# Optimization experiments

Hardware: AMD Instinct MI355X
Metric: run time of the kernel (lower is better)

The kernel has to match this reference:

```python
import jax, jax.numpy as jnp
import numpy as np

B, T, D_K, N_HEADS, D_FF, VOCAB, N_LAYERS = 4, 1024, 1024, 16, 4096, 65, 6


def setup_inputs() -> dict:
    key = jax.random.key(0)
    ks = jax.random.split(key, 12)
    f = lambda k, sh: jax.random.normal(k, sh, dtype=jnp.float32) * 0.02
    return {
        "batchData": jax.random.randint(ks[0], (B, T), 0, VOCAB),
        "target": jax.random.randint(ks[1], (B, T), 0, VOCAB),
        "pos": jnp.arange(T),
        "Wtok": f(ks[2], (VOCAB, D_K)),
        "Wpos": f(ks[3], (T, D_K)),
        "Wq": f(ks[4], (D_K, D_K)), "bq": jnp.zeros((D_K,), jnp.float32),
        "Wk": f(ks[5], (D_K, D_K)), "bk": jnp.zeros((D_K,), jnp.float32),
        "Wv": f(ks[6], (D_K, D_K)), "bv": jnp.zeros((D_K,), jnp.float32),
        "W1": f(ks[7], (D_K, D_FF)), "b1": jnp.zeros((D_FF,), jnp.float32),
        "W2": f(ks[8], (D_FF, D_K)), "b2": jnp.zeros((D_K,), jnp.float32),
        "ln_w": jnp.ones((D_K,), jnp.float32),
        "Wf": f(ks[9], (D_K, VOCAB)), "bf": jnp.zeros((VOCAB,), jnp.float32),
        "n_layers": N_LAYERS,
        "n_heads": N_HEADS,
    }


def layer_norm(x, w, eps=1e-5):
    m = jnp.mean(x, axis=-1, keepdims=True)
    v = jnp.var(x, axis=-1, keepdims=True)
    return (x - m) / jnp.sqrt(v + eps) * w


def reference(batchData, target, pos, Wtok, Wpos, Wq, bq, Wk, bk, Wv, bv,
              W1, b1, W2, b2, ln_w, Wf, bf, n_layers, n_heads):
    x = Wtok[batchData] + Wpos[pos]  # [B, T, C] (pos embedding broadcasts)
    Bsz, Tlen, C = x.shape
    dh = C // n_heads
    mask = jnp.tril(jnp.ones((Tlen, Tlen), dtype=bool))
    inv_sqrt_dk = 1.0 / jnp.sqrt(jnp.float32(C))  # source divides by sqrt(full d_k)

    def block(x):
        q = (x @ Wq + bq).reshape(Bsz, Tlen, n_heads, dh).transpose(0, 2, 1, 3)
        k = (x @ Wk + bk).reshape(Bsz, Tlen, n_heads, dh).transpose(0, 2, 1, 3)
        v = (x @ Wv + bv).reshape(Bsz, Tlen, n_heads, dh).transpose(0, 2, 1, 3)
        scores = jnp.einsum('bhqd,bhkd->bhqk', q, k) * inv_sqrt_dk
        scores = jnp.where(mask, scores, -jnp.inf)
        attn = jax.nn.softmax(scores, axis=-1)
        h = jnp.einsum('bhqk,bhkd->bhqd', attn, v)
        h = h.transpose(0, 2, 1, 3).reshape(Bsz, Tlen, C)
        h = h + layer_norm(h, ln_w)           # x = x + ln(x) (shared ln)
        ff = jax.nn.relu(h @ W1 + b1) @ W2 + b2
        return ff + layer_norm(ff, ln_w)      # same shared ln again

    # ModuleList repeats the SAME block object, so weights are shared across layers
    for _ in range(n_layers):
        x = block(x)

    logits = x @ Wf + bf                       # [B, T, V]
    probs = jax.nn.softmax(logits, axis=1)     # softmax over T, as in source
    pred = probs.reshape(Bsz * Tlen, -1)
    onehot = jax.nn.one_hot(target.reshape(-1), VOCAB, dtype=jnp.float32)
    # F.cross_entropy with soft (one-hot float) targets
    loss = -jnp.mean(jnp.sum(onehot * jax.nn.log_softmax(pred, axis=-1), axis=-1))
    return loss, probs
```

## Files before the change

kernel.cpp:

```cpp
#include <hip/hip_runtime.h>

typedef __attribute__((ext_vector_type(8))) short bh8;
typedef __attribute__((ext_vector_type(4))) float f4v;

constexpr int VOC = 65;
constexpr int NL  = 6;
constexpr int Mrow = 4096;

__device__ inline float b2f(unsigned short u) {
  union { unsigned int i; float f; } x; x.i = ((unsigned int)u) << 16; return x.f;
}
__device__ inline unsigned short f2b(float f) {
  union { float f; unsigned int i; } x; x.f = f;
  return (unsigned short)((x.i + 0x7FFFu + ((x.i >> 16) & 1u)) >> 16);
}
__device__ inline void gld16(const void* g, void* l) {
  __builtin_amdgcn_global_load_lds(
      (const __attribute__((address_space(1))) unsigned int*)g,
      (__attribute__((address_space(3))) unsigned int*)l, 16, 0, 0);
}
__device__ inline bh8 lds_swz(const unsigned short* base, int row, int colbyte) {
  int off = row * 128 + (colbyte ^ ((row & 7) << 4));
  return *(const bh8*)((const char*)base + off);
}
__device__ inline f4v mfma16(bh8 a, bh8 b, f4v c) {
  return __builtin_amdgcn_mfma_f32_16x16x32_bf16(a, b, c, 0, 0, 0);
}
#define WAITV(n) asm volatile("s_waitcnt vmcnt(" #n ")" ::: "memory")
template <int N> __device__ inline void waitvl() {
  if constexpr (N == 0)
    asm volatile("s_waitcnt vmcnt(0) lgkmcnt(0)" ::: "memory");
  else if constexpr (N == 3)
    asm volatile("s_waitcnt vmcnt(3) lgkmcnt(0)" ::: "memory");
  else if constexpr (N == 4)
    asm volatile("s_waitcnt vmcnt(4) lgkmcnt(0)" ::: "memory");
  else
    asm volatile("s_waitcnt vmcnt(6) lgkmcnt(0)" ::: "memory");
}

__global__ __launch_bounds__(256) void wt_conv(const float* __restrict__ src,
    unsigned short* __restrict__ dst, int K, int N) {
  __shared__ float t[32][33];
  int k0 = blockIdx.x * 32, n0 = blockIdx.y * 32;
  int tid = threadIdx.x;
#pragma unroll
  for (int i = 0; i < 4; ++i) {
    int idx = tid + i * 256;
    int kr = idx >> 5, nc = idx & 31;
    t[kr][nc] = (n0 + nc < N) ? src[(size_t)(k0 + kr) * N + n0 + nc] : 0.f;
  }
  __syncthreads();
#pragma unroll
  for (int i = 0; i < 4; ++i) {
    int idx = tid + i * 256;
    int nr = idx >> 5, kc = idx & 31;
    dst[(size_t)(n0 + nr) * K + k0 + kc] = f2b(t[kc][nr]);
  }
}

__global__ __launch_bounds__(256) void bias_prep(
    const float* __restrict__ bq, const float* __restrict__ bk,
    const float* __restrict__ bv, const float* __restrict__ bf,
    float* __restrict__ bqkv, float* __restrict__ bfp) {
  int i = blockIdx.x * 256 + threadIdx.x;
  if (i < 1024) bqkv[i] = bq[i];
  else if (i < 2048) bqkv[i] = bk[i - 1024];
  else if (i < 3072) bqkv[i] = bv[i - 2048];
  else if (i < 3200) bfp[i - 3072] = (i - 3072 < VOC) ? bf[i - 3072] : 0.f;
}

__global__ __launch_bounds__(256) void embed_bf(const int* __restrict__ tok,
    const float* __restrict__ Wtok, const float* __restrict__ Wpos,
    unsigned short* __restrict__ Xb) {
  int bt = blockIdx.x, t = bt & 1023, tid = threadIdx.x;
  int id = tok[bt];
  float4 a = ((const float4*)(Wtok + (size_t)id * 1024))[tid];
  float4 p = ((const float4*)(Wpos + (size_t)t * 1024))[tid];
  ushort4 o;
  o.x = f2b(a.x + p.x); o.y = f2b(a.y + p.y);
  o.z = f2b(a.z + p.z); o.w = f2b(a.w + p.w);
  ((ushort4*)(Xb + (size_t)bt * 1024))[tid] = o;
}

template <int BM, bool RELU, bool PART, bool VT>
__global__ __launch_bounds__((BM == 256 ? 512 : 256)) void gemm8(
    const unsigned short* __restrict__ A, const unsigned short* __restrict__ Bt,
    const float* __restrict__ bias, void* __restrict__ Cout,
    unsigned short* __restrict__ Vtout, long N, long Kloop, long lda, long ldb,
    int MT, int NT, int CM, int CN) {
  constexpr int T = (BM == 256 ? 512 : 256);
  constexpr int RPL = T / 4;
  constexpr int LA = BM / RPL, LB = 128 / RPL;
  constexpr int LNUM = LA + LB;
  __shared__ unsigned short As[3 * BM * 32];
  __shared__ unsigned short Bs[3 * 128 * 32];
  const int tid = threadIdx.x;
  const int lane = tid & 63, w = tid >> 6;
  const int wr = w >> 1, wc = w & 1;
  const int lr = lane & 15, lh = lane >> 4, lh4 = lh * 4;

  const int x = (int)blockIdx.x & 7, j = (int)blockIdx.x >> 3;
  const int gM = MT / CM;
  const int rowT = (x % gM) * CM + (j % CM);
  const int c = (x / gM) * CN + (j / CM);
  const int colT = c % NT, ksl = c / NT;
  const long row0 = (long)rowT * BM, col0 = (long)colT * 128;
  const long kOff = (long)ksl * Kloop;

  f4v acc[4][4];
#pragma unroll
  for (int i = 0; i < 4; ++i)
#pragma unroll
    for (int jj = 0; jj < 4; ++jj) acc[i][jj] = f4v{0.f, 0.f, 0.f, 0.f};

  const int rg = tid >> 2, s = tid & 3;
  const int ch = s ^ ((rg ^ (rg >> 2)) & 3);
  const unsigned short* Ap = A + (row0 + rg) * lda + kOff + ch * 8;
  const unsigned short* Bp = Bt + (col0 + rg) * ldb + kOff + ch * 8;

  auto stage = [&](int t, int buf) {
    const long k0 = (long)t << 5;
#pragma unroll
    for (int i = 0; i < LA; ++i)
      gld16(Ap + (long)i * RPL * lda + k0, &As[buf * BM * 32 + (i * T + tid) * 8]);
#pragma unroll
    for (int i = 0; i < LB; ++i)
      gld16(Bp + (long)i * RPL * ldb + k0, &Bs[buf * 4096 + (i * T + tid) * 8]);
  };

  const int nt = (int)(Kloop >> 5);
  stage(0, 0);
  stage(1, 1);

  const int fl = (lr ^ (lr >> 2)) & 3;
  const int slot = lh ^ fl;

  for (int t = 0; t < nt; ++t) {
    if (t + 1 < nt) { waitvl<LNUM>(); } else { waitvl<0>(); }
    __builtin_amdgcn_s_barrier();
    __builtin_amdgcn_sched_barrier(0);
    const unsigned short* Ab = &As[(t % 3) * BM * 32];
    const unsigned short* Bb = &Bs[(t % 3) * 4096];
    bh8 a[4], b[4];
#pragma unroll
    for (int mi = 0; mi < 4; ++mi)
      a[mi] = *(const bh8*)&Ab[(wr * 64 + mi * 16 + lr) * 32 + slot * 8];
#pragma unroll
    for (int ni = 0; ni < 4; ++ni)
      b[ni] = *(const bh8*)&Bb[(wc * 64 + ni * 16 + lr) * 32 + slot * 8];
    if (t + 2 < nt) stage(t + 2, (t + 2) % 3);
    __builtin_amdgcn_s_setprio(1);
#pragma unroll
    for (int mi = 0; mi < 4; ++mi)
#pragma unroll
      for (int ni = 0; ni < 4; ++ni)
        acc[mi][ni] = mfma16(a[mi], b[ni], acc[mi][ni]);
    __builtin_amdgcn_s_setprio(0);
  }

  if (PART) {
    unsigned short* P = (unsigned short*)Cout + (size_t)ksl * 4096 * 1024;
#pragma unroll
    for (int mi = 0; mi < 4; ++mi)
#pragma unroll
      for (int ni = 0; ni < 4; ++ni) {
        long col = col0 + wc * 64 + ni * 16 + lr;
#pragma unroll
        for (int r = 0; r < 4; ++r) {
          long row = row0 + wr * 64 + mi * 16 + lh4 + r;
          P[row * N + col] = f2b(acc[mi][ni][r]);
        }
      }
    return;
  }
  if (VT && col0 >= 2048) {
#pragma unroll
    for (int mi = 0; mi < 4; ++mi) {
#pragma unroll
      for (int ni = 0; ni < 4; ++ni) {
        int col = (int)col0 + wc * 64 + ni * 16 + lr;
        float bb = bias[col];
        int cc = col - 2048;
        long row = row0 + wr * 64 + mi * 16 + lh4;
        int bi = (int)(row >> 10), tt = (int)(row & 1023);
        ushort4 o;
        o.x = f2b(acc[mi][ni][0] + bb);
        o.y = f2b(acc[mi][ni][1] + bb);
        o.z = f2b(acc[mi][ni][2] + bb);
        o.w = f2b(acc[mi][ni][3] + bb);
        *(ushort4*)&Vtout[((size_t)(bi * 16 + (cc >> 6)) * 64 + (cc & 63)) *
                              1024 + tt] = o;
      }
    }
    return;
  }
  const float qsc = (VT && col0 < 1024) ? 0.03125f : 1.0f;
#pragma unroll
  for (int mi = 0; mi < 4; ++mi) {
#pragma unroll
    for (int ni = 0; ni < 4; ++ni) {
      long col = col0 + wc * 64 + ni * 16 + lr;
      float bb = bias[col];
#pragma unroll
      for (int r = 0; r < 4; ++r) {
        long row = row0 + wr * 64 + mi * 16 + lh4 + r;
        float v = acc[mi][ni][r] + bb;
        if (VT) v *= qsc;
        if (RELU) v = fmaxf(v, 0.f);
        ((unsigned short*)Cout)[row * N + col] = f2b(v);
      }
    }
  }
}

template <int TM, int TN, bool RELU, bool F32OUT>
__global__ __launch_bounds__(256) void gemm4(
    const unsigned short* __restrict__ A, const unsigned short* __restrict__ Bt,
    const float* __restrict__ bias, void* __restrict__ Cout, long N, long K) {
  constexpr int MI = TM / 32, NI = TN / 32;
  constexpr int ABUF = TM * 64, BBUF = TN * 64;
  __shared__ unsigned short As[2 * ABUF];
  __shared__ unsigned short Bs[2 * BBUF];
  const int tid = threadIdx.x;
  const int lane = tid & 63, w = tid >> 6;
  const int wr = w >> 1, wc = w & 1;
  const int lr = lane & 15, lh = lane >> 4, lh4 = lh * 4;
  const long row0 = (long)blockIdx.x * TM, col0 = (long)blockIdx.y * TN;
  f4v acc[MI][NI];
#pragma unroll
  for (int i = 0; i < MI; ++i)
#pragma unroll
    for (int j = 0; j < NI; ++j) acc[i][j] = f4v{0.f, 0.f, 0.f, 0.f};
  const int rg = tid >> 3, s = tid & 7;
  const int ch = s ^ (rg & 7);
  const unsigned short* Ap = A + (row0 + rg) * K + ch * 8;
  const unsigned short* Bp = Bt + (col0 + rg) * K + ch * 8;
  auto stage = [&](int t, int buf) {
    const long k0 = (long)t << 6;
#pragma unroll
    for (int i = 0; i < MI; ++i)
      gld16(Ap + i * 32 * K + k0, &As[buf * ABUF + (i * 256 + tid) * 8]);
#pragma unroll
    for (int i = 0; i < NI; ++i)
      gld16(Bp + i * 32 * K + k0, &Bs[buf * BBUF + (i * 256 + tid) * 8]);
  };
  const int nt = (int)(K >> 6);
  stage(0, 0);
  for (int t = 0; t < nt; ++t) {
    const int cur = t & 1;
    if (t + 1 < nt) {
      stage(t + 1, cur ^ 1);
      WAITV(6);
    } else {
      WAITV(0);
    }
    __builtin_amdgcn_s_barrier();
    const unsigned short* Ab = &As[cur * ABUF];
    const unsigned short* Bb = &Bs[cur * BBUF];
#pragma unroll
    for (int ks = 0; ks < 2; ++ks) {
      bh8 a[MI], b[NI];
      const int slot = ((ks << 2) | lh) ^ (lr & 7);
#pragma unroll
      for (int mi = 0; mi < MI; ++mi) {
        int m = wr * (TM / 2) + mi * 16 + lr;
        a[mi] = *(const bh8*)((const char*)Ab + m * 128 + slot * 16);
      }
#pragma unroll
      for (int ni = 0; ni < NI; ++ni) {
        int n = wc * (TN / 2) + ni * 16 + lr;
        b[ni] = *(const bh8*)((const char*)Bb + n * 128 + slot * 16);
      }
#pragma unroll
      for (int mi = 0; mi < MI; ++mi)
#pragma unroll
        for (int ni = 0; ni < NI; ++ni)
          acc[mi][ni] = mfma16(a[mi], b[ni], acc[mi][ni]);
    }
    __builtin_amdgcn_s_barrier();
  }
#pragma unroll
  for (int mi = 0; mi < MI; ++mi) {
#pragma unroll
    for (int ni = 0; ni < NI; ++ni) {
      long col = col0 + wc * (TN / 2) + ni * 16 + lr;
      float bb = bias[col];
#pragma unroll
      for (int r = 0; r < 4; ++r) {
        long row = row0 + wr * (TM / 2) + mi * 16 + lh4 + r;
        float v = acc[mi][ni][r] + bb;
        if (RELU) v = fmaxf(v, 0.f);
        if (F32OUT) ((float*)Cout)[row * N + col] = v;
        else ((unsigned short*)Cout)[row * N + col] = f2b(v);
      }
    }
  }
}

__global__ __launch_bounds__(256) void attn_mfma(
    const unsigned short* __restrict__ QKV, const unsigned short* __restrict__ Vt,
    unsigned short* __restrict__ Hout) {
  __shared__ unsigned short Ks[2][64 * 64];
  __shared__ unsigned short Vs[2][64 * 64];
  __shared__ unsigned short Ps[4][16 * 64];
  const int tid = threadIdx.x, w = tid >> 6, lane = tid & 63;
  const int wid = ((int)blockIdx.x & 7) * 128 + ((int)blockIdx.x >> 3);
  const int bh = wid >> 4;
  const int qt = 15 - (wid & 15);
  const int b = bh >> 4, h = bh & 15;
  const int lr = lane & 15, lh = lane >> 4, lh4 = lh * 4;

  const unsigned short* qp =
      QKV + (size_t)(b * 1024 + qt * 64 + w * 16 + lr) * 3072 + h * 64 + lh * 8;
  bh8 aq0 = *(const bh8*)qp;
  bh8 aq1 = *(const bh8*)(qp + 32);

  f4v o[4];
#pragma unroll
  for (int i = 0; i < 4; ++i) o[i] = f4v{0.f, 0.f, 0.f, 0.f};
  float m = -1e30f, l = 0.f;

  const int r8 = tid >> 3, slot = tid & 7;
  unsigned short* pw = &Ps[w][0];

  auto stage = [&](int kt, int buf) {
    int r = r8, c8 = (slot ^ (r & 7)) * 8;
    gld16(QKV + (size_t)(b * 1024 + kt * 64 + r) * 3072 + 1024 + h * 64 + c8,
          &Ks[buf][tid * 8]);
    gld16(Vt + (size_t)(bh * 64 + r) * 1024 + kt * 64 + c8, &Vs[buf][tid * 8]);
    r = r8 + 32; c8 = (slot ^ (r & 7)) * 8;
    gld16(QKV + (size_t)(b * 1024 + kt * 64 + r) * 3072 + 1024 + h * 64 + c8,
          &Ks[buf][2048 + tid * 8]);
    gld16(Vt + (size_t)(bh * 64 + r) * 1024 + kt * 64 + c8,
          &Vs[buf][2048 + tid * 8]);
  };

  stage(0, 0);

  for (int kt = 0; kt <= qt; ++kt) {
    const int cur = kt & 1;
    if (kt < qt) {
      stage(kt + 1, cur ^ 1);
      WAITV(4);
    } else {
      WAITV(0);
    }
    __builtin_amdgcn_s_barrier();

    f4v s[4];
#pragma unroll
    for (int nt = 0; nt < 4; ++nt) {
      bh8 k0 = lds_swz(Ks[cur], nt * 16 + lr, lh * 16);
      bh8 k1 = lds_swz(Ks[cur], nt * 16 + lr, lh * 16 + 64);
      f4v z = f4v{0.f, 0.f, 0.f, 0.f};
      z = mfma16(k0, aq0, z);
      z = mfma16(k1, aq1, z);
      s[nt] = z;
    }
    const bool diag = (kt == qt);
    if (diag) {
      const int qloc = w * 16 + lr;
#pragma unroll
      for (int nt = 0; nt < 4; ++nt)
#pragma unroll
        for (int r = 0; r < 4; ++r)
          if ((nt * 16 + lh4 + r) > qloc) s[nt][r] = -1e30f;
    }
    float tm = fmaxf(fmaxf(fmaxf(s[0][0], s[0][1]), fmaxf(s[0][2], s[0][3])),
                     fmaxf(fmaxf(s[1][0], s[1][1]), fmaxf(s[1][2], s[1][3])));
    float tm2 = fmaxf(fmaxf(fmaxf(s[2][0], s[2][1]), fmaxf(s[2][2], s[2][3])),
                      fmaxf(fmaxf(s[3][0], s[3][1]), fmaxf(s[3][2], s[3][3])));
    tm = fmaxf(tm, tm2);
    tm = fmaxf(tm, __shfl_xor(tm, 16));
    tm = fmaxf(tm, __shfl_xor(tm, 32));

    const bool resc = __any(tm > m + 8.f);
    const float mu = resc ? fmaxf(m, tm) : m;
    float sum = 0.f;
#pragma unroll
    for (int nt = 0; nt < 4; ++nt)
#pragma unroll
      for (int r = 0; r < 4; ++r) {
        float e = __expf(s[nt][r] - mu);
        s[nt][r] = e;
        sum += e;
      }
    sum += __shfl_xor(sum, 16);
    sum += __shfl_xor(sum, 32);
    if (resc) {
      float corr = __expf(m - mu);
      m = mu;
      l = l * corr + sum;
      float c0 = __shfl(corr, lh4 + 0), c1 = __shfl(corr, lh4 + 1);
      float c2 = __shfl(corr, lh4 + 2), c3 = __shfl(corr, lh4 + 3);
#pragma unroll
      for (int nt = 0; nt < 4; ++nt) {
        o[nt][0] *= c0; o[nt][1] *= c1; o[nt][2] *= c2; o[nt][3] *= c3;
      }
    } else {
      l += sum;
    }
#pragma unroll
    for (int nt = 0; nt < 4; ++nt) {
      unsigned int u0, u1;
      asm("v_cvt_pk_bf16_f32 %0, %1, %2" : "=v"(u0) : "v"(s[nt][0]), "v"(s[nt][1]));
      asm("v_cvt_pk_bf16_f32 %0, %1, %2" : "=v"(u1) : "v"(s[nt][2]), "v"(s[nt][3]));
      uint2 pk{u0, u1};
      *(uint2*)((char*)pw + lr * 128 + ((nt * 32 + lh * 8) ^ ((lr & 7) << 4))) = pk;
    }
    bh8 pa0 = lds_swz(pw, lr, lh * 16);
    bh8 pa1 = lds_swz(pw, lr, lh * 16 + 64);
#pragma unroll
    for (int nt = 0; nt < 4; ++nt) {
      bh8 v0 = lds_swz(Vs[cur], nt * 16 + lr, lh * 16);
      bh8 v1 = lds_swz(Vs[cur], nt * 16 + lr, lh * 16 + 64);
      o[nt] = mfma16(pa0, v0, o[nt]);
      o[nt] = mfma16(pa1, v1, o[nt]);
    }
    __builtin_amdgcn_s_barrier();
  }
  float linv = 1.f / l;
  float l0 = __shfl(linv, lh4 + 0), l1 = __shfl(linv, lh4 + 1);
  float l2 = __shfl(linv, lh4 + 2), l3 = __shfl(linv, lh4 + 3);
  const size_t rowb = (size_t)(b * 1024 + qt * 64 + w * 16);
#pragma unroll
  for (int nt = 0; nt < 4; ++nt) {
    int col = h * 64 + nt * 16 + lr;
    Hout[(rowb + lh4 + 0) * 1024 + col] = f2b(o[nt][0] * l0);
    Hout[(rowb + lh4 + 1) * 1024 + col] = f2b(o[nt][1] * l1);
    Hout[(rowb + lh4 + 2) * 1024 + col] = f2b(o[nt][2] * l2);
    Hout[(rowb + lh4 + 3) * 1024 + col] = f2b(o[nt][3] * l3);
  }
}

__global__ __launch_bounds__(256) void ln_res_bf(
    const unsigned short* __restrict__ Xi, const float* __restrict__ wln,
    unsigned short* __restrict__ Y) {
  int row = blockIdx.x, tid = threadIdx.x;
  ushort4 u = ((const ushort4*)(Xi + (size_t)row * 1024))[tid];
  float x0 = b2f(u.x), x1 = b2f(u.y), x2 = b2f(u.z), x3 = b2f(u.w);
  float s = x0 + x1 + x2 + x3;
  float ss = x0 * x0 + x1 * x1 + x2 * x2 + x3 * x3;
#pragma unroll
  for (int off = 32; off; off >>= 1) {
    s += __shfl_xor(s, off);
    ss += __shfl_xor(ss, off);
  }
  __shared__ float sw[4], ssw[4];
  int wv = tid >> 6, ln = tid & 63;
  if (ln == 0) { sw[wv] = s; ssw[wv] = ss; }
  __syncthreads();
  s = sw[0] + sw[1] + sw[2] + sw[3];
  ss = ssw[0] + ssw[1] + ssw[2] + ssw[3];
  float mean = s * (1.f / 1024.f);
  float var = ss * (1.f / 1024.f) - mean * mean;
  float rstd = rsqrtf(var + 1e-5f);
  float4 wv4 = ((const float4*)wln)[tid];
  ushort4 out;
  out.x = f2b(x0 + (x0 - mean) * rstd * wv4.x);
  out.y = f2b(x1 + (x1 - mean) * rstd * wv4.y);
  out.z = f2b(x2 + (x2 - mean) * rstd * wv4.z);
  out.w = f2b(x3 + (x3 - mean) * rstd * wv4.w);
  ((ushort4*)(Y + (size_t)row * 1024))[tid] = out;
}

__global__ __launch_bounds__(256) void ln2_fuse(
    const unsigned short* __restrict__ P, const float* __restrict__ b2,
    const float* __restrict__ wln, unsigned short* __restrict__ Y) {
  int row = blockIdx.x, tid = threadIdx.x;
  const size_t plane = (size_t)4096 * 1024;
  float x0 = 0.f, x1 = 0.f, x2 = 0.f, x3 = 0.f;
#pragma unroll
  for (int pl = 0; pl < 4; ++pl) {
    ushort4 u = *(const ushort4*)&P[pl * plane + (size_t)row * 1024 + tid * 4];
    x0 += b2f(u.x); x1 += b2f(u.y); x2 += b2f(u.z); x3 += b2f(u.w);
  }
  float4 bb = ((const float4*)b2)[tid];
  x0 += bb.x; x1 += bb.y; x2 += bb.z; x3 += bb.w;
  float s = x0 + x1 + x2 + x3;
  float ss = x0 * x0 + x1 * x1 + x2 * x2 + x3 * x3;
#pragma unroll
  for (int off = 32; off; off >>= 1) {
    s += __shfl_xor(s, off);
    ss += __shfl_xor(ss, off);
  }
  __shared__ float sw[4], ssw[4];
  int wv = tid >> 6, ln = tid & 63;
  if (ln == 0) { sw[wv] = s; ssw[wv] = ss; }
  __syncthreads();
  s = sw[0] + sw[1] + sw[2] + sw[3];
  ss = ssw[0] + ssw[1] + ssw[2] + ssw[3];
  float mean = s * (1.f / 1024.f);
  float var = ss * (1.f / 1024.f) - mean * mean;
  float rstd = rsqrtf(var + 1e-5f);
  float4 wv4 = ((const float4*)wln)[tid];
  ushort4 out;
  out.x = f2b(x0 + (x0 - mean) * rstd * wv4.x);
  out.y = f2b(x1 + (x1 - mean) * rstd * wv4.y);
  out.z = f2b(x2 + (x2 - mean) * rstd * wv4.z);
  out.w = f2b(x3 + (x3 - mean) * rstd * wv4.w);
  ((ushort4*)(Y + (size_t)row * 1024))[tid] = out;
}

__global__ __launch_bounds__(256) void softmaxT_kernel(
    const float* __restrict__ logits, float* __restrict__ probs) {
  int b = blockIdx.x / VOC;
  int v = blockIdx.x - b * VOC;
  const float* src = logits + (size_t)b * 1024 * 128 + v;
  float vals[4];
  float m = -1e30f;
#pragma unroll
  for (int i = 0; i < 4; ++i) {
    int t = threadIdx.x + 256 * i;
    vals[i] = src[(size_t)t * 128];
    m = fmaxf(m, vals[i]);
  }
#pragma unroll
  for (int off = 32; off; off >>= 1) m = fmaxf(m, __shfl_xor(m, off));
  __shared__ float sm[4], ssum[4];
  int wv = threadIdx.x >> 6, ln = threadIdx.x & 63;
  if (ln == 0) sm[wv] = m;
  __syncthreads();
  m = fmaxf(fmaxf(sm[0], sm[1]), fmaxf(sm[2], sm[3]));
  float s = 0.f;
#pragma unroll
  for (int i = 0; i < 4; ++i) { vals[i] = __expf(vals[i] - m); s += vals[i]; }
#pragma unroll
  for (int off = 32; off; off >>= 1) s += __shfl_xor(s, off);
  if (ln == 0) ssum[wv] = s;
  __syncthreads();
  s = ssum[0] + ssum[1] + ssum[2] + ssum[3];
  float inv = 1.f / s;
  float* dst = probs + (size_t)b * 1024 * VOC + v;
#pragma unroll
  for (int i = 0; i < 4; ++i) {
    int t = threadIdx.x + 256 * i;
    dst[(size_t)t * VOC] = vals[i] * inv;
  }
}

__global__ __launch_bounds__(256) void loss_rows_kernel(
    const float* __restrict__ probs, const int* __restrict__ tgt,
    float* __restrict__ partial) {
  int wv = threadIdx.x >> 6, lane = threadIdx.x & 63;
  int row = blockIdx.x * 4 + wv;
  const float* p = probs + (size_t)row * VOC;
  float x0 = p[lane];
  float x1 = (lane == 0) ? p[64] : -1e30f;
  float m = fmaxf(x0, x1);
#pragma unroll
  for (int off = 32; off; off >>= 1) m = fmaxf(m, __shfl_xor(m, off));
  float s = __expf(x0 - m) + ((lane == 0) ? __expf(x1 - m) : 0.f);
#pragma unroll
  for (int off = 32; off; off >>= 1) s += __shfl_xor(s, off);
  if (lane == 0) {
    int tg = tgt[row];
    partial[row] = (p[tg] - m) - logf(s);
  }
}

__global__ __launch_bounds__(256) void loss_final_kernel(
    const float* __restrict__ partial, float* __restrict__ out) {
  float s = 0.f;
  for (int i = threadIdx.x; i < Mrow; i += 256) s += partial[i];
#pragma unroll
  for (int off = 32; off; off >>= 1) s += __shfl_xor(s, off);
  __shared__ float sw[4];
  int wv = threadIdx.x >> 6, ln = threadIdx.x & 63;
  if (ln == 0) sw[wv] = s;
  __syncthreads();
  if (threadIdx.x == 0) out[0] = -(sw[0] + sw[1] + sw[2] + sw[3]) / (float)Mrow;
}

extern "C" void kernel_launch(void* const* d_in, const int* in_sizes, int n_in,
                              void* d_out, int out_size, void* d_ws,
                              size_t ws_size, hipStream_t stream) {
  (void)in_sizes; (void)n_in; (void)out_size; (void)ws_size;
  const int*   tok    = (const int*)d_in[0];
  const int*   target = (const int*)d_in[1];
  const float* Wtok   = (const float*)d_in[3];
  const float* Wpos   = (const float*)d_in[4];
  const float* Wq = (const float*)d_in[5];  const float* bq = (const float*)d_in[6];
  const float* Wk = (const float*)d_in[7];  const float* bk = (const float*)d_in[8];
  const float* Wv = (const float*)d_in[9];  const float* bv = (const float*)d_in[10];
  const float* W1 = (const float*)d_in[11]; const float* b1 = (const float*)d_in[12];
  const float* W2 = (const float*)d_in[13]; const float* b2 = (const float*)d_in[14];
  const float* lnw = (const float*)d_in[15];
  const float* Wf = (const float*)d_in[16]; const float* bf = (const float*)d_in[17];
  float* out = (float*)d_out;

  char* p = (char*)d_ws;
  unsigned short* Xb    = (unsigned short*)p; p += (size_t)Mrow * 1024 * 2;
  unsigned short* QKVb  = (unsigned short*)p; p += (size_t)Mrow * 3072 * 2;
  unsigned short* Vt    = (unsigned short*)p; p += (size_t)64 * 64 * 1024 * 2;
  unsigned short* Hb    = (unsigned short*)p; p += (size_t)Mrow * 1024 * 2;
  unsigned short* F2b   = (unsigned short*)p; p += (size_t)Mrow * 1024 * 2;
  unsigned short* FF1b  = (unsigned short*)p; p += (size_t)Mrow * 4096 * 2;
  unsigned short* WqkvT = (unsigned short*)p; p += (size_t)3072 * 1024 * 2;
  unsigned short* W1T   = (unsigned short*)p; p += (size_t)4096 * 1024 * 2;
  unsigned short* W2T   = (unsigned short*)p; p += (size_t)1024 * 4096 * 2;
  unsigned short* WfT   = (unsigned short*)p; p += (size_t)128 * 1024 * 2;
  float* bqkv = (float*)p; p += 3072 * 4;
  float* bfp  = (float*)p; p += 128 * 4;
  float* LOG  = (float*)p; p += (size_t)Mrow * 128 * 4;
  float* PART = (float*)p; p += Mrow * 4;
  unsigned short* Pff2 = QKVb;

  wt_conv<<<dim3(32, 32), 256, 0, stream>>>(Wq, WqkvT,                1024, 1024);
  wt_conv<<<dim3(32, 32), 256, 0, stream>>>(Wk, WqkvT + 1024 * 1024,  1024, 1024);
  wt_conv<<<dim3(32, 32), 256, 0, stream>>>(Wv, WqkvT + 2048 * 1024,  1024, 1024);
  wt_conv<<<dim3(32, 128), 256, 0, stream>>>(W1, W1T, 1024, 4096);
  wt_conv<<<dim3(128, 32), 256, 0, stream>>>(W2, W2T, 4096, 1024);
  wt_conv<<<dim3(32, 4), 256, 0, stream>>>(Wf, WfT, 1024, VOC);
  bias_prep<<<13, 256, 0, stream>>>(bq, bk, bv, bf, bqkv, bfp);

  embed_bf<<<Mrow, 256, 0, stream>>>(tok, Wtok, Wpos, Xb);

  for (int l = 0; l < NL; ++l) {
    gemm8<128, false, false, true><<<768, 256, 0, stream>>>(
        Xb, WqkvT, bqkv, QKVb, Vt, 3072, 1024, 1024, 1024, 32, 24, 8, 12);
    attn_mfma<<<1024, 256, 0, stream>>>(QKVb, Vt, Hb);
    ln_res_bf<<<Mrow, 256, 0, stream>>>(Hb, lnw, F2b);
    gemm8<256, true, false, false><<<512, 512, 0, stream>>>(
        F2b, W1T, b1, FF1b, nullptr, 4096, 1024, 1024, 1024, 16, 32, 8, 8);
    gemm8<256, false, true, false><<<512, 512, 0, stream>>>(
        FF1b, W2T, nullptr, Pff2, nullptr, 1024, 1024, 4096, 4096, 16, 8, 8, 8);
    ln2_fuse<<<Mrow, 256, 0, stream>>>(Pff2, b2, lnw, Xb);
  }

  gemm4<64, 128, false, true><<<dim3(64, 1), 256, 0, stream>>>(
      Xb, WfT, bfp, LOG, 128, 1024);
  softmaxT_kernel<<<4 * VOC, 256, 0, stream>>>(LOG, out + 1);
  loss_rows_kernel<<<Mrow / 4, 256, 0, stream>>>(out + 1, target, PART);
  loss_final_kernel<<<1, 256, 0, stream>>>(PART, out);
}
```

Before: 1.019 ms.

## Replace GEMM kernels with 256x256 tile, BK=64 ping-pong quadrant-scheduled kernel

```diff
diff --git a/kernel.cpp b/kernel.cpp
--- a/kernel.cpp
+++ b/kernel.cpp
@@ -27,16 +27,10 @@
   return __builtin_amdgcn_mfma_f32_16x16x32_bf16(a, b, c, 0, 0, 0);
 }
 #define WAITV(n) asm volatile("s_waitcnt vmcnt(" #n ")" ::: "memory")
-template <int N> __device__ inline void waitvl() {
-  if constexpr (N == 0)
-    asm volatile("s_waitcnt vmcnt(0) lgkmcnt(0)" ::: "memory");
-  else if constexpr (N == 3)
-    asm volatile("s_waitcnt vmcnt(3) lgkmcnt(0)" ::: "memory");
-  else if constexpr (N == 4)
-    asm volatile("s_waitcnt vmcnt(4) lgkmcnt(0)" ::: "memory");
-  else
-    asm volatile("s_waitcnt vmcnt(6) lgkmcnt(0)" ::: "memory");
-}
+#define LGKM0 asm volatile("s_waitcnt lgkmcnt(0)" ::: "memory")
+#define LGKM8 asm volatile("s_waitcnt lgkmcnt(8)" ::: "memory")
+#define SBAR0 __builtin_amdgcn_sched_barrier(0)
+#define BAR __builtin_amdgcn_s_barrier()
 
 __global__ __launch_bounds__(256) void wt_conv(const float* __restrict__ src,
     unsigned short* __restrict__ dst, int K, int N) {
@@ -82,21 +76,16 @@
   ((ushort4*)(Xb + (size_t)bt * 1024))[tid] = o;
 }
 
-template <int BM, bool RELU, bool PART, bool VT>
-__global__ __launch_bounds__((BM == 256 ? 512 : 256)) void gemm8(
+template <bool RELU, bool PART, bool VT>
+__global__ __launch_bounds__(512, 1) void gemm256(
     const unsigned short* __restrict__ A, const unsigned short* __restrict__ Bt,
     const float* __restrict__ bias, void* __restrict__ Cout,
     unsigned short* __restrict__ Vtout, long N, long Kloop, long lda, long ldb,
     int MT, int NT, int CM, int CN) {
-  constexpr int T = (BM == 256 ? 512 : 256);
-  constexpr int RPL = T / 4;
-  constexpr int LA = BM / RPL, LB = 128 / RPL;
-  constexpr int LNUM = LA + LB;
-  __shared__ unsigned short As[3 * BM * 32];
-  __shared__ unsigned short Bs[3 * 128 * 32];
-  const int tid = threadIdx.x;
-  const int lane = tid & 63, w = tid >> 6;
-  const int wr = w >> 1, wc = w & 1;
+  __shared__ unsigned short Abuf[2][256 * 64];
+  __shared__ unsigned short Bbuf[2][256 * 64];
+  const int tid = threadIdx.x, lane = tid & 63, w = tid >> 6;
+  const int wr = w >> 2, wc = w & 3;
   const int lr = lane & 15, lh = lane >> 4, lh4 = lh * 4;
 
   const int x = (int)blockIdx.x & 7, j = (int)blockIdx.x >> 3;
@@ -104,70 +93,140 @@
   const int rowT = (x % gM) * CM + (j % CM);
   const int c = (x / gM) * CN + (j / CM);
   const int colT = c % NT, ksl = c / NT;
-  const long row0 = (long)rowT * BM, col0 = (long)colT * 128;
+  const long row0 = (long)rowT * 256, col0 = (long)colT * 256;
   const long kOff = (long)ksl * Kloop;
 
-  f4v acc[4][4];
-#pragma unroll
-  for (int i = 0; i < 4; ++i)
+  f4v acc[8][4];
+#pragma unroll
+  for (int i = 0; i < 8; ++i)
 #pragma unroll
     for (int jj = 0; jj < 4; ++jj) acc[i][jj] = f4v{0.f, 0.f, 0.f, 0.f};
 
-  const int rg = tid >> 2, s = tid & 3;
-  const int ch = s ^ ((rg ^ (rg >> 2)) & 3);
+  const int rg = tid >> 3, sIdx = tid & 7;
+  const int ch = sIdx ^ (rg & 7);
   const unsigned short* Ap = A + (row0 + rg) * lda + kOff + ch * 8;
   const unsigned short* Bp = Bt + (col0 + rg) * ldb + kOff + ch * 8;
 
-  auto stage = [&](int t, int buf) {
-    const long k0 = (long)t << 5;
-#pragma unroll
-    for (int i = 0; i < LA; ++i)
-      gld16(Ap + (long)i * RPL * lda + k0, &As[buf * BM * 32 + (i * T + tid) * 8]);
-#pragma unroll
-    for (int i = 0; i < LB; ++i)
-      gld16(Bp + (long)i * RPL * ldb + k0, &Bs[buf * 4096 + (i * T + tid) * 8]);
+  auto stA = [&](int t, int h) {
+    const long k0 = (long)t << 6;
+#pragma unroll
+    for (int i = 0; i < 2; ++i)
+      gld16(Ap + (long)(h * 128 + i * 64) * lda + k0,
+            &Abuf[t & 1][(h * 128 + i * 64) * 64 + tid * 8]);
   };
-
-  const int nt = (int)(Kloop >> 5);
-  stage(0, 0);
-  stage(1, 1);
-
-  const int fl = (lr ^ (lr >> 2)) & 3;
-  const int slot = lh ^ fl;
+  auto stB = [&](int t, int h) {
+    const long k0 = (long)t << 6;
+#pragma unroll
+    for (int i = 0; i < 2; ++i)
+      gld16(Bp + (long)(h * 128 + i * 64) * ldb + k0,
+            &Bbuf[t & 1][(h * 128 + i * 64) * 64 + tid * 8]);
+  };
+
+  const int nt = (int)(Kloop >> 6);
+  stA(0, 0); stA(0, 1); stB(0, 0); stB(0, 1);
+  stA(1, 0); stA(1, 1); stB(1, 0);
+  WAITV(6);
+  BAR;
+
+  const int sl0 = (lh ^ (lr & 7)) * 8;
+  const int sl1 = ((4 + lh) ^ (lr & 7)) * 8;
 
   for (int t = 0; t < nt; ++t) {
-    if (t + 1 < nt) { waitvl<LNUM>(); } else { waitvl<0>(); }
-    __builtin_amdgcn_s_barrier();
-    __builtin_amdgcn_sched_barrier(0);
-    const unsigned short* Ab = &As[(t % 3) * BM * 32];
-    const unsigned short* Bb = &Bs[(t % 3) * 4096];
-    bh8 a[4], b[4];
+    const unsigned short* Ab = Abuf[t & 1];
+    const unsigned short* Bb = Bbuf[t & 1];
+    bh8 a0[4][2], a1[4][2], b0[2][2], b1[2][2];
+#pragma unroll
+    for (int mi = 0; mi < 4; ++mi) {
+      const int row = (2 * mi + wr) * 16 + lr;
+      a0[mi][0] = *(const bh8*)&Ab[row * 64 + sl0];
+      a0[mi][1] = *(const bh8*)&Ab[row * 64 + sl1];
+    }
+#pragma unroll
+    for (int ni = 0; ni < 2; ++ni) {
+      const int row = (4 * ni + wc) * 16 + lr;
+      b0[ni][0] = *(const bh8*)&Bb[row * 64 + sl0];
+      b0[ni][1] = *(const bh8*)&Bb[row * 64 + sl1];
+    }
+    if (t + 1 < nt) stB(t + 1, 1);
+    LGKM8;
+    BAR;
+    LGKM0; SBAR0;
+    __builtin_amdgcn_s_setprio(1);
 #pragma unroll
     for (int mi = 0; mi < 4; ++mi)
-      a[mi] = *(const bh8*)&Ab[(wr * 64 + mi * 16 + lr) * 32 + slot * 8];
-#pragma unroll
-    for (int ni = 0; ni < 4; ++ni)
-      b[ni] = *(const bh8*)&Bb[(wc * 64 + ni * 16 + lr) * 32 + slot * 8];
-    if (t + 2 < nt) stage(t + 2, (t + 2) % 3);
+#pragma unroll
+      for (int ni = 0; ni < 2; ++ni) {
+        acc[mi][ni] = mfma16(a0[mi][0], b0[ni][0], acc[mi][ni]);
+        acc[mi][ni] = mfma16(a0[mi][1], b0[ni][1], acc[mi][ni]);
+      }
+    __builtin_amdgcn_s_setprio(0);
+    BAR;
+#pragma unroll
+    for (int mi = 0; mi < 4; ++mi) {
+      const int row = (2 * (mi + 4) + wr) * 16 + lr;
+      a1[mi][0] = *(const bh8*)&Ab[row * 64 + sl0];
+      a1[mi][1] = *(const bh8*)&Ab[row * 64 + sl1];
+    }
+    if (t + 2 < nt) stA(t + 2, 0);
+    BAR;
+    LGKM0; SBAR0;
     __builtin_amdgcn_s_setprio(1);
 #pragma unroll
     for (int mi = 0; mi < 4; ++mi)
 #pragma unroll
-      for (int ni = 0; ni < 4; ++ni)
-        acc[mi][ni] = mfma16(a[mi], b[ni], acc[mi][ni]);
+      for (int ni = 0; ni < 2; ++ni) {
+        acc[mi + 4][ni] = mfma16(a1[mi][0], b0[ni][0], acc[mi + 4][ni]);
+        acc[mi + 4][ni] = mfma16(a1[mi][1], b0[ni][1], acc[mi + 4][ni]);
+      }
     __builtin_amdgcn_s_setprio(0);
+    BAR;
+#pragma unroll
+    for (int ni = 0; ni < 2; ++ni) {
+      const int row = (4 * (ni + 2) + wc) * 16 + lr;
+      b1[ni][0] = *(const bh8*)&Bb[row * 64 + sl0];
+      b1[ni][1] = *(const bh8*)&Bb[row * 64 + sl1];
+    }
+    if (t + 2 < nt) stA(t + 2, 1);
+    BAR;
+    LGKM0; SBAR0;
+    __builtin_amdgcn_s_setprio(1);
+#pragma unroll
+    for (int mi = 0; mi < 4; ++mi)
+#pragma unroll
+      for (int ni = 0; ni < 2; ++ni) {
+        acc[mi][ni + 2] = mfma16(a0[mi][0], b1[ni][0], acc[mi][ni + 2]);
+        acc[mi][ni + 2] = mfma16(a0[mi][1], b1[ni][1], acc[mi][ni + 2]);
+      }
+    __builtin_amdgcn_s_setprio(0);
+    BAR;
+    if (t + 2 < nt) stB(t + 2, 0);
+    BAR;
+    SBAR0;
+    __builtin_amdgcn_s_setprio(1);
+#pragma unroll
+    for (int mi = 0; mi < 4; ++mi)
+#pragma unroll
+      for (int ni = 0; ni < 2; ++ni) {
+        acc[mi + 4][ni + 2] = mfma16(a1[mi][0], b1[ni][0], acc[mi + 4][ni + 2]);
+        acc[mi + 4][ni + 2] = mfma16(a1[mi][1], b1[ni][1], acc[mi + 4][ni + 2]);
+      }
+    __builtin_amdgcn_s_setprio(0);
+    if (t + 1 < nt) {
+      if (t + 2 < nt) { WAITV(6); } else { WAITV(0); }
+      BAR;
+    }
   }
 
   if (PART) {
     unsigned short* P = (unsigned short*)Cout + (size_t)ksl * 4096 * 1024;
 #pragma unroll
-    for (int mi = 0; mi < 4; ++mi)
+    for (int mi = 0; mi < 8; ++mi)
 #pragma unroll
       for (int ni = 0; ni < 4; ++ni) {
-        long col = col0 + wc * 64 + ni * 16 + lr;
+        long col = col0 + (4 * ni + wc) * 16 + lr;
 #pragma unroll
         for (int r = 0; r < 4; ++r) {
-          long row = row0 + wr * 64 + mi * 16 + lh4 + r;
+          long row = row0 + (2 * mi + wr) * 16 + lh4 + r;
           P[row * N + col] = f2b(acc[mi][ni][r]);
         }
       }
@@ -175,13 +234,13 @@
   }
   if (VT && col0 >= 2048) {
 #pragma unroll
-    for (int mi = 0; mi < 4; ++mi) {
+    for (int mi = 0; mi < 8; ++mi)
 #pragma unroll
       for (int ni = 0; ni < 4; ++ni) {
-        int col = (int)col0 + wc * 64 + ni * 16 + lr;
+        int col = (int)col0 + (4 * ni + wc) * 16 + lr;
         float bb = bias[col];
         int cc = col - 2048;
-        long row = row0 + wr * 64 + mi * 16 + lh4;
+        long row = row0 + (2 * mi + wr) * 16 + lh4;
         int bi = (int)(row >> 10), tt = (int)(row & 1023);
         ushort4 o;
         o.x = f2b(acc[mi][ni][0] + bb);
@@ -191,26 +250,24 @@
         *(ushort4*)&Vtout[((size_t)(bi * 16 + (cc >> 6)) * 64 + (cc & 63)) *
                               1024 + tt] = o;
       }
-    }
     return;
   }
-  const float qsc = (VT && col0 < 1024) ? 0.03125f : 1.0f;
-#pragma unroll
-  for (int mi = 0; mi < 4; ++mi) {
+#pragma unroll
+  for (int mi = 0; mi < 8; ++mi)
 #pragma unroll
     for (int ni = 0; ni < 4; ++ni) {
-      long col = col0 + wc * 64 + ni * 16 + lr;
+      long col = col0 + (4 * ni + wc) * 16 + lr;
       float bb = bias[col];
+      const float qsc = (VT && col < 1024) ? 0.03125f : 1.0f;
 #pragma unroll
       for (int r = 0; r < 4; ++r) {
-        long row = row0 + wr * 64 + mi * 16 + lh4 + r;
+        long row = row0 + (2 * mi + wr) * 16 + lh4 + r;
         float v = acc[mi][ni][r] + bb;
         if (VT) v *= qsc;
         if (RELU) v = fmaxf(v, 0.f);
         ((unsigned short*)Cout)[row * N + col] = f2b(v);
       }
     }
-  }
 }
 
 template <int TM, int TN, bool RELU, bool F32OUT>
@@ -254,7 +311,7 @@
     } else {
       WAITV(0);
     }
-    __builtin_amdgcn_s_barrier();
+    BAR;
     const unsigned short* Ab = &As[cur * ABUF];
     const unsigned short* Bb = &Bs[cur * BBUF];
 #pragma unroll
@@ -277,7 +334,7 @@
         for (int ni = 0; ni < NI; ++ni)
           acc[mi][ni] = mfma16(a[mi], b[ni], acc[mi][ni]);
     }
-    __builtin_amdgcn_s_barrier();
+    BAR;
   }
 #pragma unroll
   for (int mi = 0; mi < MI; ++mi) {
@@ -345,7 +402,7 @@
     } else {
       WAITV(0);
     }
-    __builtin_amdgcn_s_barrier();
+    BAR;
 
     f4v s[4];
 #pragma unroll
@@ -417,7 +474,7 @@
       o[nt] = mfma16(pa0, v0, o[nt]);
       o[nt] = mfma16(pa1, v1, o[nt]);
     }
-    __builtin_amdgcn_s_barrier();
+    BAR;
   }
   float linv = 1.f / l;
   float l0 = __shfl(linv, lh4 + 0), l1 = __shfl(linv, lh4 + 1);
@@ -617,14 +674,14 @@
   embed_bf<<<Mrow, 256, 0, stream>>>(tok, Wtok, Wpos, Xb);
 
   for (int l = 0; l < NL; ++l) {
-    gemm8<128, false, false, true><<<768, 256, 0, stream>>>(
-        Xb, WqkvT, bqkv, QKVb, Vt, 3072, 1024, 1024, 1024, 32, 24, 8, 12);
+    gemm256<false, false, true><<<192, 512, 0, stream>>>(
+        Xb, WqkvT, bqkv, QKVb, Vt, 3072, 1024, 1024, 1024, 16, 12, 4, 6);
     attn_mfma<<<1024, 256, 0, stream>>>(QKVb, Vt, Hb);
     ln_res_bf<<<Mrow, 256, 0, stream>>>(Hb, lnw, F2b);
-    gemm8<256, true, false, false><<<512, 512, 0, stream>>>(
-        F2b, W1T, b1, FF1b, nullptr, 4096, 1024, 1024, 1024, 16, 32, 8, 8);
-    gemm8<256, false, true, false><<<512, 512, 0, stream>>>(
-        FF1b, W2T, nullptr, Pff2, nullptr, 1024, 1024, 4096, 4096, 16, 8, 8, 8);
+    gemm256<true, false, false><<<256, 512, 0, stream>>>(
+        F2b, W1T, b1, FF1b, nullptr, 4096, 1024, 1024, 1024, 16, 16, 4, 8);
+    gemm256<false, true, false><<<256, 512, 0, stream>>>(
+        FF1b, W2T, nullptr, Pff2, nullptr, 1024, 1024, 4096, 4096, 16, 4, 4, 8);
     ln2_fuse<<<Mrow, 256, 0, stream>>>(Pff2, b2, lnw, Xb);
   }
 
```

Measured after the change: 994.6 us. 2.4% less time.
